# Performance work log

Hardware: AMD Instinct MI355X
Metric: run time of the kernel (lower is better)

The kernel has to match this reference:

```python
import jax, jax.numpy as jnp
import numpy as np

B, T, OBS, E, H, A = 256, 128, 512, 1024, 1024, 64


def setup_inputs() -> dict:
    key = jax.random.key(0)
    ks = jax.random.split(key, 8)
    s = 0.02
    return {
        "obs": jax.random.normal(ks[0], (B, T, OBS), jnp.float32),
        "h0": jnp.zeros((B, H), jnp.float32),
        "c0": jnp.zeros((B, H), jnp.float32),
        "W1": jax.random.normal(ks[1], (OBS, E), jnp.float32) * s,
        "b1": jnp.zeros((E,), jnp.float32),
        "W2": jax.random.normal(ks[2], (E, E), jnp.float32) * s,
        "b2": jnp.zeros((E,), jnp.float32),
        "w_ih": jax.random.normal(ks[3], (4 * H, E), jnp.float32) * s,
        "w_hh": jax.random.normal(ks[4], (4 * H, H), jnp.float32) * s,
        "b_ih": jnp.zeros((4 * H,), jnp.float32).at[H:2 * H].set(1.0),  # forget-gate bias init
        "b_hh": jnp.zeros((4 * H,), jnp.float32),
        "ln_g": jnp.ones((H,), jnp.float32),
        "ln_b": jnp.zeros((H,), jnp.float32),
        "Wa": jax.random.normal(ks[5], (H, A), jnp.float32) * s,
        "ba": jnp.zeros((A,), jnp.float32),
        "Wc": jax.random.normal(ks[6], (H, 1), jnp.float32) * s,
        "bc": jnp.zeros((1,), jnp.float32),
        "Wobs": jax.random.normal(ks[7], (H, OBS), jnp.float32) * s,
        "bobs": jnp.zeros((OBS,), jnp.float32),
        "Wr": jax.random.normal(jax.random.fold_in(key, 9), (H, 1), jnp.float32) * s,
        "br": jnp.zeros((1,), jnp.float32),
    }


def _layernorm(x, g, b, eps=1e-5):
    mu = jnp.mean(x, axis=-1, keepdims=True)
    var = jnp.mean(jnp.square(x - mu), axis=-1, keepdims=True)
    return (x - mu) * jax.lax.rsqrt(var + eps) * g + b


def reference(obs, h0, c0, W1, b1, W2, b2, w_ih, w_hh, b_ih, b_hh,
              ln_g, ln_b, Wa, ba, Wc, bc, Wobs, bobs, Wr, br):
    # obs encoder: Linear -> SiLU -> Linear -> SiLU   [B,T,OBS] -> [B,T,E]
    enc = jax.nn.silu(jax.nn.silu(obs @ W1 + b1) @ W2 + b2)
    # precompute input contribution to gates (batched GEMM): [B,T,4H]
    gx = jnp.einsum('bte,ge->btg', enc, w_ih) + (b_ih + b_hh)
    gx_t = jnp.transpose(gx, (1, 0, 2))  # [T,B,4H] for scan

    Hs = h0.shape[-1]

    def step(carry, g_in):
        h, c = carry
        gates = g_in + h @ w_hh.T  # [B,4H]
        i = jax.nn.sigmoid(gates[:, :Hs])
        f = jax.nn.sigmoid(gates[:, Hs:2 * Hs])
        g = jnp.tanh(gates[:, 2 * Hs:3 * Hs])
        o = jax.nn.sigmoid(gates[:, 3 * Hs:])
        new_c = f * c + i * g
        new_h = o * jnp.tanh(new_c)
        return (new_h, new_c), new_h

    (hT, cT), h_seq = jax.lax.scan(step, (h0, c0), gx_t)  # h_seq: [T,B,H]
    h_seq = jnp.transpose(h_seq, (1, 0, 2))  # [B,T,H] batch-first internal format

    x = _layernorm(h_seq, ln_g, ln_b)
    logits = x @ Wa + ba            # [B,T,A]
    values = x @ Wc + bc            # [B,T,1]
    obs_pred = x @ Wobs + bobs      # [B,T,OBS]
    rew_pred = x @ Wr + br          # [B,T,1]
    return (logits, values, obs_pred, rew_pred, hT, cT)
```

## Files before the change

### kernel.cpp

```cpp
#include <hip/hip_runtime.h>
#include <cstdint>

constexpr int Bb = 256, Tt = 128, OBSn = 512, Ee = 1024, Hh = 1024, Aa = 64;
constexpr int Tc = 16;

typedef __attribute__((ext_vector_type(8))) short bf16x8;
typedef __attribute__((ext_vector_type(4))) float floatx4;

__device__ __forceinline__ unsigned short f2bf(float f) {
  union { float f; unsigned u; } c; c.f = f;
  unsigned r = c.u + 0x7fffu + ((c.u >> 16) & 1u);
  return (unsigned short)(r >> 16);
}
__device__ __forceinline__ float bf2f(unsigned short h) {
  union { unsigned u; float f; } c; c.u = ((unsigned)h) << 16; return c.f;
}
__device__ __forceinline__ void gload16(const void* g, void* l) {
  __builtin_amdgcn_global_load_lds(
      (__attribute__((address_space(1))) void*)(uintptr_t)g,
      (__attribute__((address_space(3))) void*)l, 16, 0, 0);
}
__device__ __forceinline__ float sigmoidf_(float x) { return 1.f / (1.f + __expf(-x)); }
__device__ __forceinline__ float tanhf_(float x) { return 2.f / (1.f + __expf(-2.f * x)) - 1.f; }

template <int EPI>
__global__ __launch_bounds__(256) void gemm_bt(
    const unsigned short* __restrict__ A, const unsigned short* __restrict__ Bt,
    const float* __restrict__ bias, void* __restrict__ Cout,
    int M, int N, int K, int ldo, int nreal) {
  __shared__ __align__(16) unsigned short sm[4][128 * 32];
  const int tid = threadIdx.x;
  const int wave = tid >> 6, lane = tid & 63;
  const int quad = lane >> 4, l16 = lane & 15;
  const int m0 = blockIdx.x * 128, n0 = blockIdx.y * 128;
  const int wm = (wave >> 1) * 64, wn = (wave & 1) * 64;

  floatx4 zero = {0.f, 0.f, 0.f, 0.f};
  floatx4 acc[4][4];
#pragma unroll
  for (int i = 0; i < 4; ++i)
#pragma unroll
    for (int j = 0; j < 4; ++j) acc[i][j] = zero;

  const int nk = K >> 5;
  auto stage = [&](int p, int k0) {
#pragma unroll
    for (int r = 0; r < 2; ++r) {
      const int cb = (r * 4 + wave) * 64;
      const int c = cb + lane;
      const int row = c >> 2, kp = (c & 3) << 3;
      gload16(A + (size_t)(m0 + row) * K + k0 + kp, &sm[p][cb * 8]);
      gload16(Bt + (size_t)(n0 + row) * K + k0 + kp, &sm[2 + p][cb * 8]);
    }
  };
  stage(0, 0);
  for (int kt = 0; kt < nk; ++kt) {
    __syncthreads();
    if (kt + 1 < nk) stage((kt + 1) & 1, (kt + 1) << 5);
    const int p = kt & 1;
    bf16x8 af[4], bfr[4];
#pragma unroll
    for (int i = 0; i < 4; ++i)
      af[i] = *(const bf16x8*)&sm[p][(wm + i * 16 + l16) * 32 + quad * 8];
#pragma unroll
    for (int i = 0; i < 4; ++i)
      bfr[i] = *(const bf16x8*)&sm[2 + p][(wn + i * 16 + l16) * 32 + quad * 8];
#pragma unroll
    for (int i = 0; i < 4; ++i)
#pragma unroll
      for (int j = 0; j < 4; ++j)
        acc[i][j] = __builtin_amdgcn_mfma_f32_16x16x32_bf16(af[i], bfr[j], acc[i][j], 0, 0, 0);
  }

  if (EPI == 3) {
#pragma unroll
    for (int i = 0; i < 4; ++i) {
#pragma unroll
      for (int j = 0; j < 4; ++j) {
        const int col = n0 + wn + j * 16 + l16;
#pragma unroll
        for (int r = 0; r < 4; ++r) {
          const int row = m0 + wm + i * 16 + quad * 4 + r;
          float v = acc[i][j][r];
          if (col < nreal) {
            v += bias[col];
            ((float*)Cout)[(size_t)row * ldo + col] = v;
          }
        }
      }
    }
  } else {
    __syncthreads();
    unsigned short* Cs = &sm[0][0];
#pragma unroll
    for (int i = 0; i < 4; ++i) {
#pragma unroll
      for (int j = 0; j < 4; ++j) {
        const int coll = wn + j * 16 + l16;
#pragma unroll
        for (int r = 0; r < 4; ++r) {
          const int rowl = wm + i * 16 + quad * 4 + r;
          float v = acc[i][j][r];
          if (EPI == 0 || EPI == 1) {
            v += bias[n0 + coll];
            v = v * sigmoidf_(v);
          }
          Cs[rowl * 128 + coll] = f2bf(v);
        }
      }
    }
    __syncthreads();
#pragma unroll
    for (int pp = 0; pp < 8; ++pp) {
      const int idx = pp * 2048 + tid * 8;
      const int rowl = idx >> 7, coll = idx & 127;
      const bf16x8 val = *(const bf16x8*)&Cs[idx];
      size_t orow;
      if (EPI == 1) {
        const int grow = m0 + rowl;
        orow = (size_t)((grow & (Tt - 1)) * Bb + (grow >> 7));
      } else {
        orow = (size_t)(m0 + rowl);
      }
      *(bf16x8*)((unsigned short*)Cout + orow * ldo + n0 + coll) = val;
    }
  }
}

__global__ __launch_bounds__(256) void lstm_step(
    const unsigned short* __restrict__ hprev, long long hstride,
    const unsigned short* __restrict__ whh,
    const unsigned short* __restrict__ gxt,
    const float* __restrict__ bias4h,
    float* __restrict__ c_st, float* __restrict__ hTf,
    unsigned short* __restrict__ hseq_t,
    int write_hT) {
  __shared__ __align__(16) unsigned short As[2][4][64 * 32];
  __shared__ __align__(16) unsigned short Bs[2][4][64 * 32];
  const int bid = blockIdx.x;
  const int xcd = bid & 7, slot = bid >> 3;
  const int m0 = (slot & 3) * 64;
  const int nh0 = (xcd + ((slot >> 2) << 3)) * 16;
  const int tid = threadIdx.x;
  const int wave = tid >> 6, lane = tid & 63;
  const int quad = lane >> 4, l16 = lane & 15;

  floatx4 zero = {0.f, 0.f, 0.f, 0.f};
  floatx4 acc[4] = {zero, zero, zero, zero};

  const int row = tid >> 2, kp = (tid & 3) << 3;
  const int wrow = ((row >> 4) << 10) + nh0 + (row & 15);
  const unsigned short* asrc = hprev + (size_t)(m0 + row) * hstride + kp;
  const unsigned short* bsrc = whh + (size_t)wrow * Hh + kp;

  auto stage = [&](int p, int k0) {
#pragma unroll
    for (int s = 0; s < 4; ++s) {
      gload16(asrc + k0 + s * 32, &As[p][s][wave * 512]);
      gload16(bsrc + k0 + s * 32, &Bs[p][s][wave * 512]);
    }
  };
  stage(0, 0);
  for (int kt = 0; kt < 8; ++kt) {
    __syncthreads();
    if (kt + 1 < 8) stage((kt + 1) & 1, (kt + 1) << 7);
    const int p = kt & 1;
#pragma unroll
    for (int s = 0; s < 4; ++s) {
      bf16x8 af = *(const bf16x8*)&As[p][s][(wave * 16 + l16) * 32 + quad * 8];
#pragma unroll
      for (int g = 0; g < 4; ++g) {
        bf16x8 bfr = *(const bf16x8*)&Bs[p][s][(g * 16 + l16) * 32 + quad * 8];
        acc[g] = __builtin_amdgcn_mfma_f32_16x16x32_bf16(af, bfr, acc[g], 0, 0, 0);
      }
    }
  }
  const int col = nh0 + l16;
#pragma unroll
  for (int r = 0; r < 4; ++r) {
    const int b = m0 + wave * 16 + quad * 4 + r;
    float pre[4];
#pragma unroll
    for (int g = 0; g < 4; ++g)
      pre[g] = acc[g][r] + bf2f(gxt[(size_t)b * 4096 + (g << 10) + col]) + bias4h[(g << 10) + col];
    const float ig = sigmoidf_(pre[0]);
    const float fg = sigmoidf_(pre[1]);
    const float gg = tanhf_(pre[2]);
    const float og = sigmoidf_(pre[3]);
    const size_t idx = (size_t)b * Hh + col;
    const float cn = fg * c_st[idx] + ig * gg;
    c_st[idx] = cn;
    const float hn = og * tanhf_(cn);
    if (write_hT) hTf[idx] = hn;
    hseq_t[(size_t)b * (Tt * Hh) + col] = f2bf(hn);
  }
}

__global__ __launch_bounds__(256) void ln_head(
    const unsigned short* __restrict__ hseq, const float* __restrict__ g,
    const float* __restrict__ b, const float* __restrict__ Wc, const float* __restrict__ bc,
    const float* __restrict__ Wr, const float* __restrict__ br,
    unsigned short* __restrict__ xout, float* __restrict__ vout, float* __restrict__ rout) {
  const int row = blockIdx.x;
  const int tid = threadIdx.x;
  const int wave = tid >> 6, lane = tid & 63;
  __shared__ float red[4][4];
  const ushort4 hv = ((const ushort4*)(hseq + (size_t)row * Hh))[tid];
  float h[4] = {bf2f(hv.x), bf2f(hv.y), bf2f(hv.z), bf2f(hv.w)};
  float s = h[0] + h[1] + h[2] + h[3];
  float ss = h[0] * h[0] + h[1] * h[1] + h[2] * h[2] + h[3] * h[3];
#pragma unroll
  for (int o = 32; o > 0; o >>= 1) { s += __shfl_xor(s, o); ss += __shfl_xor(ss, o); }
  if (lane == 0) { red[0][wave] = s; red[1][wave] = ss; }
  __syncthreads();
  s = red[0][0] + red[0][1] + red[0][2] + red[0][3];
  ss = red[1][0] + red[1][1] + red[1][2] + red[1][3];
  const float mu = s * (1.f / 1024.f);
  const float var = ss * (1.f / 1024.f) - mu * mu;
  const float rs = rsqrtf(var + 1e-5f);
  const float4 gv = ((const float4*)g)[tid];
  const float4 bv = ((const float4*)b)[tid];
  const float4 wcv = ((const float4*)Wc)[tid];
  const float4 wrv = ((const float4*)Wr)[tid];
  const float x0 = (h[0] - mu) * rs * gv.x + bv.x;
  const float x1 = (h[1] - mu) * rs * gv.y + bv.y;
  const float x2 = (h[2] - mu) * rs * gv.z + bv.z;
  const float x3 = (h[3] - mu) * rs * gv.w + bv.w;
  ushort4 pk; pk.x = f2bf(x0); pk.y = f2bf(x1); pk.z = f2bf(x2); pk.w = f2bf(x3);
  ((ushort4*)(xout + (size_t)row * Hh))[tid] = pk;
  float v = x0 * wcv.x + x1 * wcv.y + x2 * wcv.z + x3 * wcv.w;
  float r = x0 * wrv.x + x1 * wrv.y + x2 * wrv.z + x3 * wrv.w;
#pragma unroll
  for (int o = 32; o > 0; o >>= 1) { v += __shfl_xor(v, o); r += __shfl_xor(r, o); }
  if (lane == 0) { red[2][wave] = v; red[3][wave] = r; }
  __syncthreads();
  if (tid == 0) {
    vout[row] = red[2][0] + red[2][1] + red[2][2] + red[2][3] + bc[0];
    rout[row] = red[3][0] + red[3][1] + red[3][2] + red[3][3] + br[0];
  }
}

__global__ __launch_bounds__(256) void cvt_bf16x4(const float4* __restrict__ in,
                                                  ushort4* __restrict__ out, int n4) {
  const int i = blockIdx.x * 256 + threadIdx.x;
  if (i < n4) {
    const float4 v = in[i];
    ushort4 o; o.x = f2bf(v.x); o.y = f2bf(v.y); o.z = f2bf(v.z); o.w = f2bf(v.w);
    out[i] = o;
  }
}
__global__ __launch_bounds__(256) void transpose_cvt(const float* __restrict__ in,
                                                     unsigned short* __restrict__ out,
                                                     int K, int N, int NPAD) {
  __shared__ float tile[32][33];
  const int tx = threadIdx.x & 31, ty = threadIdx.x >> 5;
  const int k0 = blockIdx.x * 32, n0 = blockIdx.y * 32;
#pragma unroll
  for (int i = 0; i < 32; i += 8) {
    const int k = k0 + ty + i, n = n0 + tx;
    tile[ty + i][tx] = (n < N && k < K) ? in[(size_t)k * N + n] : 0.f;
  }
  __syncthreads();
#pragma unroll
  for (int i = 0; i < 32; i += 8) {
    const int n = n0 + ty + i, k = k0 + tx;
    if (n < NPAD && k < K) out[(size_t)n * K + k] = f2bf(tile[tx][ty + i]);
  }
}
__global__ __launch_bounds__(256) void prep_kernel(
    const float* __restrict__ b_ih, const float* __restrict__ b_hh, float* __restrict__ bias4h,
    const float* __restrict__ h0, const float* __restrict__ c0,
    unsigned short* __restrict__ h0bf, float* __restrict__ c_st) {
  const int i = blockIdx.x * 256 + threadIdx.x;
  if (i < 4096) bias4h[i] = b_ih[i] + b_hh[i];
  h0bf[i] = f2bf(h0[i]);
  c_st[i] = c0[i];
}
__global__ __launch_bounds__(256) void copy_hc(const float* __restrict__ h,
                                               const float* __restrict__ c,
                                               float* __restrict__ oh, float* __restrict__ oc) {
  const int i = blockIdx.x * 256 + threadIdx.x;
  oh[i] = h[i];
  oc[i] = c[i];
}

constexpr size_t SZ_W1T = (size_t)Ee * OBSn * 2;
constexpr size_t SZ_W2T = (size_t)Ee * Ee * 2;
constexpr size_t SZ_WAT = (size_t)128 * Hh * 2;
constexpr size_t SZ_WOBST = (size_t)OBSn * Hh * 2;
constexpr size_t SZ_WIH = (size_t)4 * Hh * Ee * 2;
constexpr size_t SZ_WHH = (size_t)4 * Hh * Hh * 2;
constexpr size_t SZ_BIAS = 4096 * 4;
constexpr size_t SZ_H0BF = (size_t)Bb * Hh * 2;
constexpr size_t SZ_CST = (size_t)Bb * Hh * 4;
constexpr size_t SZ_HTF = (size_t)Bb * Hh * 4;
constexpr size_t SZ_R1 = (size_t)Bb * Tt * OBSn * 2;
constexpr size_t SZ_R2 = (size_t)Bb * Tt * Ee * 2;

constexpr size_t OFF_W1T = 0;
constexpr size_t OFF_W2T = OFF_W1T + SZ_W1T;
constexpr size_t OFF_WAT = OFF_W2T + SZ_W2T;
constexpr size_t OFF_WOBST = OFF_WAT + SZ_WAT;
constexpr size_t OFF_WIH = OFF_WOBST + SZ_WOBST;
constexpr size_t OFF_WHH = OFF_WIH + SZ_WIH;
constexpr size_t OFF_BIAS = OFF_WHH + SZ_WHH;
constexpr size_t OFF_H0BF = OFF_BIAS + SZ_BIAS;
constexpr size_t OFF_CST = OFF_H0BF + SZ_H0BF;
constexpr size_t OFF_HTF = OFF_CST + SZ_CST;
constexpr size_t OFF_R1 = OFF_HTF + SZ_HTF;
constexpr size_t OFF_R2 = OFF_R1 + SZ_R1;
constexpr size_t WS_NEED = OFF_R2 + SZ_R2;

constexpr size_t OFF_LOGITS = 0;
constexpr size_t OFF_V = (size_t)Bb * Tt * Aa;
constexpr size_t OFF_OBS = OFF_V + (size_t)Bb * Tt;
constexpr size_t OFF_R = OFF_OBS + (size_t)Bb * Tt * OBSn;
constexpr size_t OFF_HT = OFF_R + (size_t)Bb * Tt;
constexpr size_t OFF_CT = OFF_HT + (size_t)Bb * Hh;

extern "C" void kernel_launch(void* const* d_in, const int* in_sizes, int n_in,
                              void* d_out, int out_size, void* d_ws, size_t ws_size,
                              hipStream_t stream) {
  if (ws_size < WS_NEED) return;

  const float* obs = (const float*)d_in[0];
  const float* h0 = (const float*)d_in[1];
  const float* c0 = (const float*)d_in[2];
  const float* W1 = (const float*)d_in[3];
  const float* b1 = (const float*)d_in[4];
  const float* W2 = (const float*)d_in[5];
  const float* b2 = (const float*)d_in[6];
  const float* w_ih = (const float*)d_in[7];
  const float* w_hh = (const float*)d_in[8];
  const float* b_ih = (const float*)d_in[9];
  const float* b_hh = (const float*)d_in[10];
  const float* ln_g = (const float*)d_in[11];
  const float* ln_b = (const float*)d_in[12];
  const float* Wa = (const float*)d_in[13];
  const float* ba = (const float*)d_in[14];
  const float* Wc = (const float*)d_in[15];
  const float* bc = (const float*)d_in[16];
  const float* Wobs = (const float*)d_in[17];
  const float* bobs = (const float*)d_in[18];
  const float* Wr = (const float*)d_in[19];
  const float* br = (const float*)d_in[20];

  char* ws = (char*)d_ws;
  unsigned short* w1t = (unsigned short*)(ws + OFF_W1T);
  unsigned short* w2t = (unsigned short*)(ws + OFF_W2T);
  unsigned short* wat = (unsigned short*)(ws + OFF_WAT);
  unsigned short* wobst = (unsigned short*)(ws + OFF_WOBST);
  unsigned short* wih = (unsigned short*)(ws + OFF_WIH);
  unsigned short* whh = (unsigned short*)(ws + OFF_WHH);
  float* bias4h = (float*)(ws + OFF_BIAS);
  unsigned short* h0bf = (unsigned short*)(ws + OFF_H0BF);
  float* cst = (float*)(ws + OFF_CST);
  float* htf = (float*)(ws + OFF_HTF);
  unsigned short* obsbf = (unsigned short*)(ws + OFF_R1);
  unsigned short* gxc = (unsigned short*)(ws + OFF_R1);
  unsigned short* enc2t = (unsigned short*)(ws + OFF_R2);
  unsigned short* xbuf = (unsigned short*)(ws + OFF_R2);
  float* out = (float*)d_out;
  unsigned short* enc1 = (unsigned short*)(out + OFF_OBS);
  unsigned short* hseq = (unsigned short*)(out + OFF_OBS);

  const dim3 blk(256);

  prep_kernel<<<dim3(1024), blk, 0, stream>>>(b_ih, b_hh, bias4h, h0, c0, h0bf, cst);
  cvt_bf16x4<<<dim3(16384), blk, 0, stream>>>((const float4*)obs, (ushort4*)obsbf, 4194304);
  cvt_bf16x4<<<dim3(4096), blk, 0, stream>>>((const float4*)w_ih, (ushort4*)wih, 1048576);
  cvt_bf16x4<<<dim3(4096), blk, 0, stream>>>((const float4*)w_hh, (ushort4*)whh, 1048576);
  transpose_cvt<<<dim3(16, 32), blk, 0, stream>>>(W1, w1t, OBSn, Ee, Ee);
  transpose_cvt<<<dim3(32, 32), blk, 0, stream>>>(W2, w2t, Ee, Ee, Ee);
  transpose_cvt<<<dim3(32, 4), blk, 0, stream>>>(Wa, wat, Hh, Aa, 128);
  transpose_cvt<<<dim3(32, 16), blk, 0, stream>>>(Wobs, wobst, Hh, OBSn, OBSn);

  gemm_bt<0><<<dim3(256, 8), blk, 0, stream>>>(obsbf, w1t, b1, enc1, 32768, Ee, OBSn, Ee, 0);
  gemm_bt<1><<<dim3(256, 8), blk, 0, stream>>>(enc1, w2t, b2, enc2t, 32768, Ee, Ee, Ee, 0);

  for (int ch = 0; ch < Tt / Tc; ++ch) {
    gemm_bt<2><<<dim3(32, 32), blk, 0, stream>>>(enc2t + (size_t)ch * Tc * Bb * Ee, wih, nullptr,
                                                 gxc, Tc * Bb, 4096, Ee, 4096, 0);
    for (int l = 0; l < Tc; ++l) {
      const int t = ch * Tc + l;
      const unsigned short* hp = (t == 0) ? h0bf : hseq + (size_t)(t - 1) * Hh;
      const long long hs = (t == 0) ? (long long)Hh : (long long)Tt * Hh;
      lstm_step<<<dim3(256), blk, 0, stream>>>(hp, hs, whh, gxc + (size_t)l * Bb * 4096,
                                               bias4h, cst, htf, hseq + (size_t)t * Hh,
                                               (t == Tt - 1) ? 1 : 0);
    }
  }

  ln_head<<<dim3(32768), blk, 0, stream>>>(hseq, ln_g, ln_b, Wc, bc, Wr, br, xbuf,
                                           out + OFF_V, out + OFF_R);
  gemm_bt<3><<<dim3(256, 1), blk, 0, stream>>>(xbuf, wat, ba, out + OFF_LOGITS, 32768, 128, Hh, Aa, Aa);
  gemm_bt<3><<<dim3(256, 4), blk, 0, stream>>>(xbuf, wobst, bobs, out + OFF_OBS, 32768, OBSn, Hh, OBSn, OBSn);
  copy_hc<<<dim3(1024), blk, 0, stream>>>(htf, cst, out + OFF_HT, out + OFF_CT);

  (void)in_sizes; (void)n_in; (void)out_size;
}
```

Measured before the change: 2.380 ms.

## Add 256x256-tile 512-thread GEMM with swizzled LDS for large matmuls

Adds a new GEMM kernel with 256x256 output tiles, 512 threads, a K-step of 64, XOR-swizzled LDS layout and XCD-aware block remapping. The encoder GEMMs, the per-chunk input-gate GEMM and the obs-prediction head now use it, while the old 128x128 kernel is kept only for the small logits head with its epilogue simplified. The larger tiles are meant to raise arithmetic intensity and cut global traffic, and the swizzle targets LDS bank conflicts. The cost is much heavier register and LDS use (128 KB shared), which lowers occupancy, and fewer workgroups for the smaller GEMMs.

```diff
diff --git a/kernel.cpp b/kernel.cpp
--- a/kernel.cpp
+++ b/kernel.cpp
@@ -22,6 +22,118 @@
 }
 __device__ __forceinline__ float sigmoidf_(float x) { return 1.f / (1.f + __expf(-x)); }
 __device__ __forceinline__ float tanhf_(float x) { return 2.f / (1.f + __expf(-2.f * x)) - 1.f; }
+
+template <int EPI>
+__global__ __launch_bounds__(512) void gemm256(
+    const unsigned short* __restrict__ A, const unsigned short* __restrict__ Bt,
+    const float* __restrict__ bias, void* __restrict__ Cout,
+    int M, int N, int K, int ldo) {
+  __shared__ __align__(16) unsigned short sm[4][256 * 64];
+  const int tid = threadIdx.x;
+  const int wave = tid >> 6, lane = tid & 63;
+  const int quad = lane >> 4, l16 = lane & 15;
+  const int nwg = gridDim.x;
+  const int wg = (blockIdx.x & 7) * (nwg >> 3) + (blockIdx.x >> 3);
+  const int nbn = N >> 8;
+  const int m0 = (wg / nbn) * 256, n0 = (wg % nbn) * 256;
+  const int wm = (wave >> 2) * 128, wn = (wave & 3) * 64;
+
+  floatx4 zero = {0.f, 0.f, 0.f, 0.f};
+  floatx4 acc[8][4];
+#pragma unroll
+  for (int i = 0; i < 8; ++i)
+#pragma unroll
+    for (int j = 0; j < 4; ++j) acc[i][j] = zero;
+
+  const int nk = K >> 6;
+  auto stage = [&](int p, int k0) {
+#pragma unroll
+    for (int s = 0; s < 4; ++s) {
+      const int c = s * 512 + tid;
+      const int row = c >> 3;
+      const int sl = (c & 7) ^ (row & 7);
+      const int lb = (s * 512 + wave * 64) * 8;
+      gload16(A + (size_t)(m0 + row) * K + k0 + sl * 8, &sm[p][lb]);
+      gload16(Bt + (size_t)(n0 + row) * K + k0 + sl * 8, &sm[2 + p][lb]);
+    }
+  };
+  stage(0, 0);
+  for (int kt = 0; kt < nk; ++kt) {
+    __syncthreads();
+    if (kt + 1 < nk) stage((kt + 1) & 1, (kt + 1) << 6);
+    const int p = kt & 1;
+#pragma unroll
+    for (int kk = 0; kk < 2; ++kk) {
+      bf16x8 af[8], bfr[4];
+#pragma unroll
+      for (int i = 0; i < 8; ++i) {
+        const int row = wm + i * 16 + l16;
+        af[i] = *(const bf16x8*)&sm[p][row * 64 + (((kk * 4 + quad) ^ (l16 & 7)) << 3)];
+      }
+#pragma unroll
+      for (int j = 0; j < 4; ++j) {
+        const int row = wn + j * 16 + l16;
+        bfr[j] = *(const bf16x8*)&sm[2 + p][row * 64 + (((kk * 4 + quad) ^ (l16 & 7)) << 3)];
+      }
+#pragma unroll
+      for (int i = 0; i < 8; ++i)
+#pragma unroll
+        for (int j = 0; j < 4; ++j)
+          acc[i][j] = __builtin_amdgcn_mfma_f32_16x16x32_bf16(af[i], bfr[j], acc[i][j], 0, 0, 0);
+    }
+  }
+
+  if (EPI == 3) {
+#pragma unroll
+    for (int i = 0; i < 8; ++i)
+#pragma unroll
+      for (int j = 0; j < 4; ++j) {
+        const int col = n0 + wn + j * 16 + l16;
+        const float bv = bias[col];
+#pragma unroll
+        for (int r = 0; r < 4; ++r) {
+          const int row = m0 + wm + i * 16 + quad * 4 + r;
+          ((float*)Cout)[(size_t)row * ldo + col] = acc[i][j][r] + bv;
+        }
+      }
+  } else {
+    __syncthreads();
+    unsigned short* Cs = &sm[0][0];
+#pragma unroll
+    for (int i = 0; i < 8; ++i)
+#pragma unroll
+      for (int j = 0; j < 4; ++j) {
+        const int coll = wn + j * 16 + l16;
+        float bv = 0.f;
+        if (EPI == 0 || EPI == 1) bv = bias[n0 + coll];
+#pragma unroll
+        for (int r = 0; r < 4; ++r) {
+          const int rowl = wm + i * 16 + quad * 4 + r;
+          float v = acc[i][j][r];
+          if (EPI == 0 || EPI == 1) {
+            v += bv;
+            v = v * sigmoidf_(v);
+          }
+          Cs[rowl * 256 + (coll ^ (quad << 4))] = f2bf(v);
+        }
+      }
+    __syncthreads();
+#pragma unroll
+    for (int pp = 0; pp < 16; ++pp) {
+      const int c2 = pp * 4096 + tid * 8;
+      const int rowl = c2 >> 8, coll = c2 & 255;
+      const bf16x8 val = *(const bf16x8*)&Cs[rowl * 256 + (coll ^ (((rowl >> 2) & 3) << 4))];
+      size_t orow;
+      if (EPI == 1) {
+        const int grow = m0 + rowl;
+        orow = (size_t)((grow & (Tt - 1)) * Bb + (grow >> 7));
+      } else {
+        orow = (size_t)(m0 + rowl);
+      }
+      *(bf16x8*)((unsigned short*)Cout + orow * ldo + n0 + coll) = val;
+    }
+  }
+}
 
 template <int EPI>
 __global__ __launch_bounds__(256) void gemm_bt(
@@ -71,58 +183,20 @@
       for (int j = 0; j < 4; ++j)
         acc[i][j] = __builtin_amdgcn_mfma_f32_16x16x32_bf16(af[i], bfr[j], acc[i][j], 0, 0, 0);
   }
-
-  if (EPI == 3) {
-#pragma unroll
-    for (int i = 0; i < 4; ++i) {
-#pragma unroll
-      for (int j = 0; j < 4; ++j) {
-        const int col = n0 + wn + j * 16 + l16;
-#pragma unroll
-        for (int r = 0; r < 4; ++r) {
-          const int row = m0 + wm + i * 16 + quad * 4 + r;
-          float v = acc[i][j][r];
-          if (col < nreal) {
-            v += bias[col];
-            ((float*)Cout)[(size_t)row * ldo + col] = v;
-          }
+#pragma unroll
+  for (int i = 0; i < 4; ++i) {
+#pragma unroll
+    for (int j = 0; j < 4; ++j) {
+      const int col = n0 + wn + j * 16 + l16;
+#pragma unroll
+      for (int r = 0; r < 4; ++r) {
+        const int row = m0 + wm + i * 16 + quad * 4 + r;
+        float v = acc[i][j][r];
+        if (col < nreal) {
+          v += bias[col];
+          ((float*)Cout)[(size_t)row * ldo + col] = v;
         }
       }
-    }
-  } else {
-    __syncthreads();
-    unsigned short* Cs = &sm[0][0];
-#pragma unroll
-    for (int i = 0; i < 4; ++i) {
-#pragma unroll
-      for (int j = 0; j < 4; ++j) {
-        const int coll = wn + j * 16 + l16;
-#pragma unroll
-        for (int r = 0; r < 4; ++r) {
-          const int rowl = wm + i * 16 + quad * 4 + r;
-          float v = acc[i][j][r];
-          if (EPI == 0 || EPI == 1) {
-            v += bias[n0 + coll];
-            v = v * sigmoidf_(v);
-          }
-          Cs[rowl * 128 + coll] = f2bf(v);
-        }
-      }
-    }
-    __syncthreads();
-#pragma unroll
-    for (int pp = 0; pp < 8; ++pp) {
-      const int idx = pp * 2048 + tid * 8;
-      const int rowl = idx >> 7, coll = idx & 127;
-      const bf16x8 val = *(const bf16x8*)&Cs[idx];
-      size_t orow;
-      if (EPI == 1) {
-        const int grow = m0 + rowl;
-        orow = (size_t)((grow & (Tt - 1)) * Bb + (grow >> 7));
-      } else {
-        orow = (size_t)(m0 + rowl);
-      }
-      *(bf16x8*)((unsigned short*)Cout + orow * ldo + n0 + coll) = val;
     }
   }
 }
@@ -365,6 +439,7 @@
   unsigned short* hseq = (unsigned short*)(out + OFF_OBS);
 
   const dim3 blk(256);
+  const dim3 blk512(512);
 
   prep_kernel<<<dim3(1024), blk, 0, stream>>>(b_ih, b_hh, bias4h, h0, c0, h0bf, cst);
   cvt_bf16x4<<<dim3(16384), blk, 0, stream>>>((const float4*)obs, (ushort4*)obsbf, 4194304);
@@ -375,12 +450,12 @@
   transpose_cvt<<<dim3(32, 4), blk, 0, stream>>>(Wa, wat, Hh, Aa, 128);
   transpose_cvt<<<dim3(32, 16), blk, 0, stream>>>(Wobs, wobst, Hh, OBSn, OBSn);
 
-  gemm_bt<0><<<dim3(256, 8), blk, 0, stream>>>(obsbf, w1t, b1, enc1, 32768, Ee, OBSn, Ee, 0);
-  gemm_bt<1><<<dim3(256, 8), blk, 0, stream>>>(enc1, w2t, b2, enc2t, 32768, Ee, Ee, Ee, 0);
+  gemm256<0><<<dim3(512), blk512, 0, stream>>>(obsbf, w1t, b1, enc1, 32768, Ee, OBSn, Ee);
+  gemm256<1><<<dim3(512), blk512, 0, stream>>>(enc1, w2t, b2, enc2t, 32768, Ee, Ee, Ee);
 
   for (int ch = 0; ch < Tt / Tc; ++ch) {
-    gemm_bt<2><<<dim3(32, 32), blk, 0, stream>>>(enc2t + (size_t)ch * Tc * Bb * Ee, wih, nullptr,
-                                                 gxc, Tc * Bb, 4096, Ee, 4096, 0);
+    gemm256<2><<<dim3(256), blk512, 0, stream>>>(enc2t + (size_t)ch * Tc * Bb * Ee, wih, nullptr,
+                                                 gxc, Tc * Bb, 4096, Ee, 4096);
     for (int l = 0; l < Tc; ++l) {
       const int t = ch * Tc + l;
       const unsigned short* hp = (t == 0) ? h0bf : hseq + (size_t)(t - 1) * Hh;
@@ -394,7 +469,7 @@
   ln_head<<<dim3(32768), blk, 0, stream>>>(hseq, ln_g, ln_b, Wc, bc, Wr, br, xbuf,
                                            out + OFF_V, out + OFF_R);
   gemm_bt<3><<<dim3(256, 1), blk, 0, stream>>>(xbuf, wat, ba, out + OFF_LOGITS, 32768, 128, Hh, Aa, Aa);
-  gemm_bt<3><<<dim3(256, 4), blk, 0, stream>>>(xbuf, wobst, bobs, out + OFF_OBS, 32768, OBSn, Hh, OBSn, OBSn);
+  gemm256<3><<<dim3(256), blk512, 0, stream>>>(xbuf, wobst, bobs, out + OFF_OBS, 32768, OBSn, Hh, OBSn);
   copy_hc<<<dim3(1024), blk, 0, stream>>>(htf, cst, out + OFF_HT, out + OFF_CT);
 
   (void)in_sizes; (void)n_in; (void)out_size;
```

Measured after the change: 2.161 ms. -9.2%, faster.
